# Performance work log

Measured on AMD Instinct MI355X. Metric: run time of the kernel, lower is better.

## Reference

```python
import jax, jax.numpy as jnp
import numpy as np

B = 65536          # batch
C = 16             # num_concepts
D = 64             # dim_per_concept
G = 32             # g_dim

def setup_inputs() -> dict:
    key = jax.random.key(0)
    ks = jax.random.split(key, 6)
    x  = jax.random.normal(ks[0], (B, C, D), dtype=jnp.float32)
    # DAG adjacency (zeros in torch init; use small random values for a nontrivial baseline)
    A  = 0.1 * jax.random.normal(ks[1], (C, C), dtype=jnp.float32)
    # Stacked per-concept 2-layer MLP weights (nets_z), torch Linear convention: W @ x + b
    W1 = jax.random.normal(ks[2], (C, G, D), dtype=jnp.float32) / np.sqrt(D)
    b1 = jax.random.normal(ks[3], (C, G), dtype=jnp.float32) * 0.01
    W2 = jax.random.normal(ks[4], (C, D, G), dtype=jnp.float32) / np.sqrt(G)
    b2 = jax.random.normal(ks[5], (C, D), dtype=jnp.float32) * 0.01
    return {"x": x, "A": A, "W1": W1, "b1": b1, "W2": W2, "b2": b2}

def reference(x, A, W1, b1, W2, b2):
    # mask: m[b,i,d] = sum_j A[j,i] * x[b,j,d]   (A.t() @ x)
    m = jnp.einsum('ji,bjd->bid', A, x)
    # g_z: per-concept Linear(D->G) -> ELU -> Linear(G->D), batched over concepts
    h = jax.nn.elu(jnp.einsum('cgd,bcd->bcg', W1, m) + b1[None, :, :])
    out = jnp.einsum('cdg,bcg->bcd', W2, h) + b2[None, :, :]
    return out  # [B, C, D]
```

## Files before the change

kernel.cpp:

```cpp
#include <hip/hip_runtime.h>
#include <hip/hip_fp16.h>

#define BATCH   65536
#define NC      16
#define DDIM    64
#define GDIM    32
#define TILE    64

extern "C" __global__ void __launch_bounds__(1024)
causal_dag_kernel(const float* __restrict__ x, const float* __restrict__ A,
                  const float* __restrict__ W1, const float* __restrict__ b1,
                  const float* __restrict__ W2, const float* __restrict__ b2,
                  float* __restrict__ out)
{
    __shared__ __align__(16) unsigned char smem_raw[65536];
    __half* xs  = (__half*)smem_raw;
    float*  osf = (float*)smem_raw;

    const int t    = threadIdx.x;
    const int b0   = blockIdx.x * TILE;
    const int w    = __builtin_amdgcn_readfirstlane(t >> 6);
    const int lane = t & 63;
    const int sw   = lane & 7;

    const float* W1c = W1 + w * (GDIM * DDIM);
    const float* W2c = W2 + w * (DDIM * GDIM);
    const float* b1c = b1 + w * GDIM;
    const float* b2c = b2 + w * DDIM;

    float m[DDIM];
#pragma unroll
    for (int d = 0; d < DDIM; ++d) m[d] = 0.f;

    for (int jh = 0; jh < 2; ++jh) {
#pragma unroll
        for (int p = 0; p < 8; ++p) {
            int f4 = p * 1024 + t;
            int bb = f4 >> 7;
            int r  = f4 & 127;
            int jp = r >> 4;
            int d4 = r & 15;
            const float4 v = *(const float4*)(
                x + ((size_t)(b0 + bb) * (NC * DDIM) + (jh * 8 + jp) * DDIM + d4 * 4));
            union { __half2 h2[2]; uint2 u; } pk;
            pk.h2[0] = __floats2half2_rn(v.x, v.y);
            pk.h2[1] = __floats2half2_rn(v.z, v.w);
            int dst = bb * 512 + jp * 64 + (((d4 >> 1) ^ (bb & 7)) << 3) + ((d4 & 1) << 2);
            *(uint2*)(xs + dst) = pk.u;
        }
        __syncthreads();

        const __half* xb = xs + lane * 512;
#pragma unroll
        for (int jp = 0; jp < 8; ++jp) {
            const float a = A[(jh * 8 + jp) * NC + w];
#pragma unroll
            for (int dq = 0; dq < 8; ++dq) {
                uint4 q = *(const uint4*)(xb + jp * 64 + ((dq ^ sw) << 3));
                const int d0 = dq * 8;
                float2 f0 = __half22float2(*(__half2*)&q.x);
                float2 f1 = __half22float2(*(__half2*)&q.y);
                float2 f2 = __half22float2(*(__half2*)&q.z);
                float2 f3 = __half22float2(*(__half2*)&q.w);
                m[d0+0] = fmaf(a, f0.x, m[d0+0]);
                m[d0+1] = fmaf(a, f0.y, m[d0+1]);
                m[d0+2] = fmaf(a, f1.x, m[d0+2]);
                m[d0+3] = fmaf(a, f1.y, m[d0+3]);
                m[d0+4] = fmaf(a, f2.x, m[d0+4]);
                m[d0+5] = fmaf(a, f2.y, m[d0+5]);
                m[d0+6] = fmaf(a, f3.x, m[d0+6]);
                m[d0+7] = fmaf(a, f3.y, m[d0+7]);
            }
        }
        if (jh == 0) __syncthreads();
    }

    float h[GDIM];
#pragma unroll
    for (int g = 0; g < GDIM; ++g) {
        float acc = b1c[g];
#pragma unroll
        for (int d = 0; d < DDIM; ++d) acc = fmaf(W1c[g * DDIM + d], m[d], acc);
        h[g] = acc > 0.f ? acc : (__expf(acc) - 1.f);
    }

    __align__(16) float o[DDIM];
#pragma unroll
    for (int d = 0; d < DDIM; ++d) {
        float acc = b2c[d];
#pragma unroll
        for (int g = 0; g < GDIM; ++g) acc = fmaf(W2c[d * GDIM + g], h[g], acc);
        o[d] = acc;
    }

    const int bl = lane & 15;
    const int lq = lane >> 4;
    for (int q = 0; q < 4; ++q) {
        __syncthreads();
        if (lq == q) {
#pragma unroll
            for (int d4 = 0; d4 < 16; ++d4) {
                int dst = bl * 1024 + w * 64 + ((d4 ^ bl) << 2);
                *(float4*)(osf + dst) = *(const float4*)(o + d4 * 4);
            }
        }
        __syncthreads();
        float4* og = (float4*)(out + (size_t)(b0 + q * 16) * (NC * DDIM));
#pragma unroll
        for (int k = 0; k < 4; ++k) {
            int f  = k * 1024 + t;
            int bb = f >> 8;
            int r  = f & 255;
            int c  = r >> 4;
            int d4 = r & 15;
            og[f] = *(const float4*)(osf + bb * 1024 + c * 64 + ((d4 ^ bb) << 2));
        }
    }
}

extern "C" void kernel_launch(void* const* d_in, const int* in_sizes, int n_in,
                              void* d_out, int out_size, void* d_ws, size_t ws_size,
                              hipStream_t stream) {
    const float* x  = (const float*)d_in[0];
    const float* A  = (const float*)d_in[1];
    const float* W1 = (const float*)d_in[2];
    const float* b1 = (const float*)d_in[3];
    const float* W2 = (const float*)d_in[4];
    const float* b2 = (const float*)d_in[5];
    float* out = (float*)d_out;

    causal_dag_kernel<<<BATCH / TILE, 1024, 0, stream>>>(x, A, W1, b1, W2, b2, out);
}
```

Baseline: 1.399 ms.

## Fuse W1 projection into mask accumulation and request higher occupancy

Replaces the 64-float mask accumulator with a 32-float hidden accumulator. Each 8-wide chunk of the mask is folded into the W1 projection as soon as it is computed, which cuts live registers. The launch bound now asks for 4 blocks per CU so the compiler caps register use. Because W1 is applied separately to each of the two concept halves, the W1 FMAs and scalar weight loads are doubled. The 64 KB LDS per block may still limit occupancy, and the tighter register cap risks spills.

```diff
diff --git a/kernel.cpp b/kernel.cpp
--- a/kernel.cpp
+++ b/kernel.cpp
@@ -7,7 +7,7 @@
 #define GDIM    32
 #define TILE    64
 
-extern "C" __global__ void __launch_bounds__(1024)
+extern "C" __global__ void __launch_bounds__(1024, 4)
 causal_dag_kernel(const float* __restrict__ x, const float* __restrict__ A,
                   const float* __restrict__ W1, const float* __restrict__ b1,
                   const float* __restrict__ W2, const float* __restrict__ b2,
@@ -28,9 +28,9 @@
     const float* b1c = b1 + w * GDIM;
     const float* b2c = b2 + w * DDIM;
 
-    float m[DDIM];
+    float hacc[GDIM];
 #pragma unroll
-    for (int d = 0; d < DDIM; ++d) m[d] = 0.f;
+    for (int g = 0; g < GDIM; ++g) hacc[g] = b1c[g];
 
     for (int jh = 0; jh < 2; ++jh) {
 #pragma unroll
@@ -50,46 +50,60 @@
         }
         __syncthreads();
 
+        float a[8];
+#pragma unroll
+        for (int jp = 0; jp < 8; ++jp) a[jp] = A[(jh * 8 + jp) * NC + w];
+
         const __half* xb = xs + lane * 512;
 #pragma unroll
-        for (int jp = 0; jp < 8; ++jp) {
-            const float a = A[(jh * 8 + jp) * NC + w];
+        for (int dq = 0; dq < 8; ++dq) {
+            float mc[8];
 #pragma unroll
-            for (int dq = 0; dq < 8; ++dq) {
+            for (int k = 0; k < 8; ++k) mc[k] = 0.f;
+#pragma unroll
+            for (int jp = 0; jp < 8; ++jp) {
                 uint4 q = *(const uint4*)(xb + jp * 64 + ((dq ^ sw) << 3));
-                const int d0 = dq * 8;
                 float2 f0 = __half22float2(*(__half2*)&q.x);
                 float2 f1 = __half22float2(*(__half2*)&q.y);
                 float2 f2 = __half22float2(*(__half2*)&q.z);
                 float2 f3 = __half22float2(*(__half2*)&q.w);
-                m[d0+0] = fmaf(a, f0.x, m[d0+0]);
-                m[d0+1] = fmaf(a, f0.y, m[d0+1]);
-                m[d0+2] = fmaf(a, f1.x, m[d0+2]);
-                m[d0+3] = fmaf(a, f1.y, m[d0+3]);
-                m[d0+4] = fmaf(a, f2.x, m[d0+4]);
-                m[d0+5] = fmaf(a, f2.y, m[d0+5]);
-                m[d0+6] = fmaf(a, f3.x, m[d0+6]);
-                m[d0+7] = fmaf(a, f3.y, m[d0+7]);
+                mc[0] = fmaf(a[jp], f0.x, mc[0]);
+                mc[1] = fmaf(a[jp], f0.y, mc[1]);
+                mc[2] = fmaf(a[jp], f1.x, mc[2]);
+                mc[3] = fmaf(a[jp], f1.y, mc[3]);
+                mc[4] = fmaf(a[jp], f2.x, mc[4]);
+                mc[5] = fmaf(a[jp], f2.y, mc[5]);
+                mc[6] = fmaf(a[jp], f3.x, mc[6]);
+                mc[7] = fmaf(a[jp], f3.y, mc[7]);
+            }
+            const int d0 = dq * 8;
+#pragma unroll
+            for (int g = 0; g < GDIM; ++g) {
+                float acc = hacc[g];
+                acc = fmaf(W1c[g * DDIM + d0 + 0], mc[0], acc);
+                acc = fmaf(W1c[g * DDIM + d0 + 1], mc[1], acc);
+                acc = fmaf(W1c[g * DDIM + d0 + 2], mc[2], acc);
+                acc = fmaf(W1c[g * DDIM + d0 + 3], mc[3], acc);
+                acc = fmaf(W1c[g * DDIM + d0 + 4], mc[4], acc);
+                acc = fmaf(W1c[g * DDIM + d0 + 5], mc[5], acc);
+                acc = fmaf(W1c[g * DDIM + d0 + 6], mc[6], acc);
+                acc = fmaf(W1c[g * DDIM + d0 + 7], mc[7], acc);
+                hacc[g] = acc;
             }
         }
         if (jh == 0) __syncthreads();
     }
 
-    float h[GDIM];
 #pragma unroll
-    for (int g = 0; g < GDIM; ++g) {
-        float acc = b1c[g];
-#pragma unroll
-        for (int d = 0; d < DDIM; ++d) acc = fmaf(W1c[g * DDIM + d], m[d], acc);
-        h[g] = acc > 0.f ? acc : (__expf(acc) - 1.f);
-    }
+    for (int g = 0; g < GDIM; ++g)
+        hacc[g] = hacc[g] > 0.f ? hacc[g] : (__expf(hacc[g]) - 1.f);
 
     __align__(16) float o[DDIM];
 #pragma unroll
     for (int d = 0; d < DDIM; ++d) {
         float acc = b2c[d];
 #pragma unroll
-        for (int g = 0; g < GDIM; ++g) acc = fmaf(W2c[d * GDIM + g], h[g], acc);
+        for (int g = 0; g < GDIM; ++g) acc = fmaf(W2c[d * GDIM + g], hacc[g], acc);
         o[d] = acc;
     }
 
```

Result: faster. 1.205 ms (-13.9%).

## Stage W1/W2 as fp16 in shared memory and reorder mask-loop LDS swizzle

Applied to the files above, without the earlier changes.

Instead of each wave reading its concept's W1/W2 from global memory through scalar or uniform loads, the block cooperatively converts all W1 and then all W2 to fp16 in a second 64KB shared-memory region, and the MLP reads them as 128-bit LDS vectors. The mask accumulation loop is interchanged (dq outer, jp inner), A values are hoisted into registers, and an extra jp XOR swizzle is added to spread LDS bank accesses. This doubles LDS use to 128KB per block and adds fp16 rounding of the weights and extra barriers.

```diff
diff --git a/kernel.cpp b/kernel.cpp
--- a/kernel.cpp
+++ b/kernel.cpp
@@ -7,14 +7,15 @@
 #define GDIM    32
 #define TILE    64
 
-extern "C" __global__ void __launch_bounds__(1024)
+extern "C" __global__ void __launch_bounds__(1024, 4)
 causal_dag_kernel(const float* __restrict__ x, const float* __restrict__ A,
                   const float* __restrict__ W1, const float* __restrict__ b1,
                   const float* __restrict__ W2, const float* __restrict__ b2,
                   float* __restrict__ out)
 {
-    __shared__ __align__(16) unsigned char smem_raw[65536];
+    __shared__ __align__(16) unsigned char smem_raw[131072];
     __half* xs  = (__half*)smem_raw;
+    __half* wsh = (__half*)(smem_raw + 65536);
     float*  osf = (float*)smem_raw;
 
     const int t    = threadIdx.x;
@@ -22,9 +23,8 @@
     const int w    = __builtin_amdgcn_readfirstlane(t >> 6);
     const int lane = t & 63;
     const int sw   = lane & 7;
+    const int lhi  = (lane >> 3) & 7;
 
-    const float* W1c = W1 + w * (GDIM * DDIM);
-    const float* W2c = W2 + w * (DDIM * GDIM);
     const float* b1c = b1 + w * GDIM;
     const float* b2c = b2 + w * DDIM;
 
@@ -45,51 +45,95 @@
             union { __half2 h2[2]; uint2 u; } pk;
             pk.h2[0] = __floats2half2_rn(v.x, v.y);
             pk.h2[1] = __floats2half2_rn(v.z, v.w);
-            int dst = bb * 512 + jp * 64 + (((d4 >> 1) ^ (bb & 7)) << 3) + ((d4 & 1) << 2);
+            int dst = bb * 512 + (jp ^ (bb >> 3)) * 64
+                    + (((d4 >> 1) ^ (bb & 7)) << 3) + ((d4 & 1) << 2);
             *(uint2*)(xs + dst) = pk.u;
+        }
+        if (jh == 0) {
+#pragma unroll
+            for (int p = 0; p < 8; ++p) {
+                int f4 = p * 1024 + t;
+                const float4 v = *(const float4*)(W1 + (size_t)f4 * 4);
+                union { __half2 h2[2]; uint2 u; } pk;
+                pk.h2[0] = __floats2half2_rn(v.x, v.y);
+                pk.h2[1] = __floats2half2_rn(v.z, v.w);
+                *(uint2*)(wsh + f4 * 4) = pk.u;
+            }
         }
         __syncthreads();
 
+        float a[8];
+#pragma unroll
+        for (int jp = 0; jp < 8; ++jp) a[jp] = A[(jh * 8 + jp) * NC + w];
+
         const __half* xb = xs + lane * 512;
 #pragma unroll
-        for (int jp = 0; jp < 8; ++jp) {
-            const float a = A[(jh * 8 + jp) * NC + w];
+        for (int dq = 0; dq < 8; ++dq) {
+            const int d0 = dq * 8;
 #pragma unroll
-            for (int dq = 0; dq < 8; ++dq) {
-                uint4 q = *(const uint4*)(xb + jp * 64 + ((dq ^ sw) << 3));
-                const int d0 = dq * 8;
+            for (int jp = 0; jp < 8; ++jp) {
+                uint4 q = *(const uint4*)(xb + (jp ^ lhi) * 64 + ((dq ^ sw) << 3));
                 float2 f0 = __half22float2(*(__half2*)&q.x);
                 float2 f1 = __half22float2(*(__half2*)&q.y);
                 float2 f2 = __half22float2(*(__half2*)&q.z);
                 float2 f3 = __half22float2(*(__half2*)&q.w);
-                m[d0+0] = fmaf(a, f0.x, m[d0+0]);
-                m[d0+1] = fmaf(a, f0.y, m[d0+1]);
-                m[d0+2] = fmaf(a, f1.x, m[d0+2]);
-                m[d0+3] = fmaf(a, f1.y, m[d0+3]);
-                m[d0+4] = fmaf(a, f2.x, m[d0+4]);
-                m[d0+5] = fmaf(a, f2.y, m[d0+5]);
-                m[d0+6] = fmaf(a, f3.x, m[d0+6]);
-                m[d0+7] = fmaf(a, f3.y, m[d0+7]);
+                m[d0+0] = fmaf(a[jp], f0.x, m[d0+0]);
+                m[d0+1] = fmaf(a[jp], f0.y, m[d0+1]);
+                m[d0+2] = fmaf(a[jp], f1.x, m[d0+2]);
+                m[d0+3] = fmaf(a[jp], f1.y, m[d0+3]);
+                m[d0+4] = fmaf(a[jp], f2.x, m[d0+4]);
+                m[d0+5] = fmaf(a[jp], f2.y, m[d0+5]);
+                m[d0+6] = fmaf(a[jp], f3.x, m[d0+6]);
+                m[d0+7] = fmaf(a[jp], f3.y, m[d0+7]);
             }
         }
         if (jh == 0) __syncthreads();
     }
 
+    const __half* w1w = wsh + w * (GDIM * DDIM);
     float h[GDIM];
 #pragma unroll
     for (int g = 0; g < GDIM; ++g) {
         float acc = b1c[g];
 #pragma unroll
-        for (int d = 0; d < DDIM; ++d) acc = fmaf(W1c[g * DDIM + d], m[d], acc);
+        for (int dq = 0; dq < 8; ++dq) {
+            uint4 qw = *(const uint4*)(w1w + g * DDIM + dq * 8);
+            const __half* hv = (const __half*)&qw;
+            const int d0 = dq * 8;
+#pragma unroll
+            for (int k = 0; k < 8; ++k)
+                acc = fmaf(__half2float(hv[k]), m[d0 + k], acc);
+        }
         h[g] = acc > 0.f ? acc : (__expf(acc) - 1.f);
     }
 
+    __syncthreads();
+
+#pragma unroll
+    for (int p = 0; p < 8; ++p) {
+        int f4 = p * 1024 + t;
+        const float4 v = *(const float4*)(W2 + (size_t)f4 * 4);
+        union { __half2 h2[2]; uint2 u; } pk;
+        pk.h2[0] = __floats2half2_rn(v.x, v.y);
+        pk.h2[1] = __floats2half2_rn(v.z, v.w);
+        *(uint2*)(wsh + f4 * 4) = pk.u;
+    }
+    __syncthreads();
+
+    const __half* w2w = wsh + w * (DDIM * GDIM);
     __align__(16) float o[DDIM];
 #pragma unroll
     for (int d = 0; d < DDIM; ++d) {
         float acc = b2c[d];
 #pragma unroll
-        for (int g = 0; g < GDIM; ++g) acc = fmaf(W2c[d * GDIM + g], h[g], acc);
+        for (int gq = 0; gq < 4; ++gq) {
+            uint4 qw = *(const uint4*)(w2w + d * GDIM + gq * 8);
+            const __half* hv = (const __half*)&qw;
+            const int g0 = gq * 8;
+#pragma unroll
+            for (int k = 0; k < 8; ++k)
+                acc = fmaf(__half2float(hv[k]), h[g0 + k], acc);
+        }
         o[d] = acc;
     }
 
```

New measurement: 1.216 ms. -13.1%, faster.
